# Kernel optimization log

Hardware: AMD Instinct MI355X
Metric: run time of the kernel (lower is better)

## Reference

```python
import jax, jax.numpy as jnp
import numpy as np

N = 50000      # nodes
E = 800000     # edges (avg degree 16)
IN = 128       # in_dim
OUT = 128      # out_dim
K = 4          # Chebyshev order
NEIG = 64      # num_eigs
H = 128        # eigval_hidden_dim
BN_EPS = 1e-5


def setup_inputs() -> dict:
    key = jax.random.key(0)
    ks = jax.random.split(key, 12)
    feature = jax.random.normal(ks[0], (N, IN), jnp.float32)
    # linear over concat of (K Chebyshev blocks + 1 spectral block) = (K+1)*IN
    lin_w = jax.random.normal(ks[1], ((K + 1) * IN, OUT), jnp.float32) / np.sqrt((K + 1) * IN)
    lin_b = jnp.zeros((OUT,), jnp.float32)
    # eigval_filter MLP: 1 -> H -> H -> 1 (ReLU between)
    ew0 = jax.random.normal(ks[2], (1, H), jnp.float32)
    eb0 = jnp.zeros((H,), jnp.float32)
    ew1 = jax.random.normal(ks[3], (H, H), jnp.float32) / np.sqrt(H)
    eb1 = jnp.zeros((H,), jnp.float32)
    ew2 = jax.random.normal(ks[4], (H, 1), jnp.float32) / np.sqrt(H)
    eb2 = jnp.zeros((1,), jnp.float32)
    bn_gamma = jnp.ones((OUT,), jnp.float32)
    bn_beta = jnp.zeros((OUT,), jnp.float32)
    lambda_max = jnp.ones((1,), jnp.float32)
    # cached (detached) spectral data for the graph
    evecs = jax.random.normal(ks[5], (N, NEIG), jnp.float32)
    evals = jax.random.uniform(ks[6], (NEIG,), jnp.float32)
    edge_src = jax.random.randint(ks[7], (E,), 0, N, jnp.int32).astype(jnp.int64)
    edge_dst = jax.random.randint(ks[8], (E,), 0, N, jnp.int32).astype(jnp.int64)
    return dict(feature=feature, lin_w=lin_w, lin_b=lin_b, ew0=ew0, eb0=eb0,
                ew1=ew1, eb1=eb1, ew2=ew2, eb2=eb2, bn_gamma=bn_gamma,
                bn_beta=bn_beta, lambda_max=lambda_max, evecs=evecs,
                evals=evals, edge_src=edge_src, edge_dst=edge_dst)


def reference(feature, lin_w, lin_b, ew0, eb0, ew1, eb1, ew2, eb2,
              bn_gamma, bn_beta, lambda_max, evecs, evals, edge_src, edge_dst):
    src = edge_src.astype(jnp.int32)
    dst = edge_dst.astype(jnp.int32)
    # in-degrees (messages arrive at dst) and D^-1/2, clamped at 1
    deg = jax.ops.segment_sum(jnp.ones((E,), jnp.float32), dst, num_segments=N)
    d_sqrt = jnp.clip(deg, 1.0, None) ** -0.5  # [N]
    d_sqrt = d_sqrt[:, None]                   # [N,1]

    def unn_laplacian(x):
        m = (x * d_sqrt)[src]                              # [E,IN]
        agg = jax.ops.segment_sum(m, dst, num_segments=N)  # [N,IN]
        return agg * d_sqrt

    re_norm = 2.0 / lambda_max  # broadcast scalar (per-node in dgl, constant here)

    X0 = feature
    blocks = [X0]
    h = unn_laplacian(X0)
    X1 = -re_norm * h + X0 * (re_norm - 1.0)
    blocks.append(X1)
    for _ in range(2, K):
        h = unn_laplacian(X1)
        Xi = -2.0 * re_norm * h + X1 * 2.0 * (re_norm - 1.0) - X0
        blocks.append(Xi)
        X1, X0 = Xi, X1

    # spectral filtering: evecs^T f, scale by MLP(evals), project back
    z = jax.nn.relu(evals[:, None] @ ew0 + eb0)   # [NEIG,H]
    z = jax.nn.relu(z @ ew1 + eb1)                # [NEIG,H]
    ef = z @ ew2 + eb2                            # [NEIG,1]
    hs = jnp.einsum('ne,nf->ef', evecs, feature)  # [NEIG,IN]
    hs = ef * hs
    hs = jnp.einsum('ne,ef->nf', evecs, hs)       # [N,IN]
    blocks.append(hs)

    Xt = jnp.concatenate(blocks, axis=1)          # [N,(K+1)*IN]
    out = Xt @ lin_w + lin_b                      # [N,OUT]

    # BatchNorm1d (training-mode batch statistics, biased variance)
    mu = jnp.mean(out, axis=0)
    var = jnp.mean((out - mu) ** 2, axis=0)
    out = (out - mu) * jax.lax.rsqrt(var + BN_EPS) * bn_gamma + bn_beta
    out = jax.nn.relu(out)
    # dropout p=0.0 -> identity; residual disabled
    return out
```

## Files before the change

kernel.cpp:

```cpp
#include <hip/hip_runtime.h>

#define N_NODES 50000
#define N_EDGES 800000
#define IN_F    128
#define OUT_F   128
#define NEIG    64
#define HDIM    128
#define BN_EPSF 1e-5f
#define XB_ROWS 50048
#define XB_COLS 640
#define SCAN_BLK 49
#define HSP_BLOCKS 521
#define HSP_NODES 96
#define RED_CHUNK 33
#define RED_SPLIT 16

typedef __attribute__((ext_vector_type(8))) short short8;
typedef __attribute__((ext_vector_type(4))) float floatx4;

#define OFF_XB      0
#define OFF_X1F     (XB_ROWS * XB_COLS / 2)
#define OFF_X2F     (OFF_X1F + N_NODES * IN_F)
#define OFF_WT      (OFF_X2F + N_NODES * IN_F)
#define OFF_DSQRT   (OFF_WT + 40960)
#define OFF_HS      (OFF_DSQRT + N_NODES)
#define OFF_EF      (OFF_HS + NEIG * OUT_F)
#define OFF_COLSUM  (OFF_EF + NEIG)
#define OFF_COLSQ   (OFF_COLSUM + OUT_F)
#define OFF_DEG     (OFF_COLSQ + OUT_F)
#define OFF_ROWSTART (OFF_DEG + N_NODES)
#define OFF_CSR     (OFF_ROWSTART + N_NODES + 1)
#define OFF_BSUM    (OFF_CSR + N_EDGES)
#define OFF_RANK    (OFF_BSUM + 64)

static __device__ inline unsigned short f2bf(float f) {
    union { float f; unsigned int u; } v; v.f = f;
    unsigned int r = (v.u + 0x7FFFu + ((v.u >> 16) & 1u)) >> 16;
    return (unsigned short)r;
}
static __device__ inline float bf2f(unsigned int u16) {
    union { unsigned int u; float f; } v; v.u = u16 << 16;
    return v.f;
}

__global__ __launch_bounds__(256) void k_prep(const float* __restrict__ feat,
                                              const float* __restrict__ W,
                                              unsigned short* __restrict__ Xb,
                                              unsigned short* __restrict__ Wt,
                                              int* __restrict__ deg,
                                              float* __restrict__ small) {
    int b = blockIdx.x;
    if (b < 3125) {
        int t = b * 256 + threadIdx.x;
        int n = t >> 4, c8 = (t & 15) * 8;
        float4 a = *(const float4*)&feat[n * IN_F + c8];
        float4 bb = *(const float4*)&feat[n * IN_F + c8 + 4];
        ushort4 o0, o1;
        o0.x = f2bf(a.x); o0.y = f2bf(a.y); o0.z = f2bf(a.z); o0.w = f2bf(a.w);
        o1.x = f2bf(bb.x); o1.y = f2bf(bb.y); o1.z = f2bf(bb.z); o1.w = f2bf(bb.w);
        *(ushort4*)&Xb[(size_t)n * XB_COLS + c8]     = o0;
        *(ushort4*)&Xb[(size_t)n * XB_COLS + c8 + 4] = o1;
    } else if (b < 3445) {
        int t = (b - 3125) * 256 + threadIdx.x;
        int k = t >> 7, n = t & 127;
        Wt[n * 640 + k] = f2bf(W[k * 128 + n]);
    } else {
        int i = (b - 3445) * 256 + threadIdx.x;
        if (i < N_NODES) deg[i] = 0;
        if (i < NEIG * OUT_F + NEIG + 2 * OUT_F) small[i] = 0.0f;
    }
}

__global__ void k_rank(int* __restrict__ deg, const int* __restrict__ dst,
                       int* __restrict__ rank) {
    int e = blockIdx.x * 256 + threadIdx.x;
    if (e < N_EDGES) rank[e] = atomicAdd(&deg[dst[e]], 1);
}

__global__ __launch_bounds__(1024) void k_scan1(const int* __restrict__ deg,
                                                int* __restrict__ row_start,
                                                int* __restrict__ bsum) {
    __shared__ int sd[1024];
    int i = blockIdx.x * 1024 + threadIdx.x;
    int v = (i < N_NODES) ? deg[i] : 0;
    sd[threadIdx.x] = v;
    __syncthreads();
    for (int off = 1; off < 1024; off <<= 1) {
        int t = (threadIdx.x >= off) ? sd[threadIdx.x - off] : 0;
        __syncthreads();
        sd[threadIdx.x] += t;
        __syncthreads();
    }
    if (i < N_NODES) row_start[i] = sd[threadIdx.x] - v;
    if (threadIdx.x == 1023) bsum[blockIdx.x] = sd[1023];
}

__global__ void k_scan2(int* __restrict__ bsum) {
    int t = threadIdx.x;
    int orig = (t < SCAN_BLK) ? bsum[t] : 0;
    int v = orig;
    for (int off = 1; off < 64; off <<= 1) {
        int u = __shfl_up(v, off);
        if (t >= off) v += u;
    }
    if (t < SCAN_BLK) bsum[t] = v - orig;
}

__global__ __launch_bounds__(1024) void k_scan3(const int* __restrict__ deg,
                                                int* __restrict__ row_start,
                                                const int* __restrict__ bsum,
                                                float* __restrict__ dsq) {
    int i = blockIdx.x * 1024 + threadIdx.x;
    if (i < N_NODES) {
        int r = row_start[i] + bsum[blockIdx.x];
        row_start[i] = r;
        dsq[i] = rsqrtf((float)max(deg[i], 1));
    }
    if (i == 0) row_start[N_NODES] = N_EDGES;
}

__global__ void k_csr(const int* __restrict__ src, const int* __restrict__ dst,
                      const int* __restrict__ rank, const int* __restrict__ row_start,
                      int* __restrict__ csr_src) {
    int e = blockIdx.x * 256 + threadIdx.x;
    if (e < N_EDGES) csr_src[row_start[dst[e]] + rank[e]] = src[e];
}

__global__ __launch_bounds__(256) void k_gather(const int* __restrict__ row_start,
                                                const int* __restrict__ csr_src,
                                                const float* __restrict__ dsq,
                                                const unsigned short* __restrict__ srcb,
                                                const unsigned short* __restrict__ prevb,
                                                const unsigned short* __restrict__ ppb,
                                                unsigned short* __restrict__ outb,
                                                const float* __restrict__ lm, int first) {
    int n = (blockIdx.x * 256 + threadIdx.x) >> 6;
    int lane = threadIdx.x & 63;
    if (n >= N_NODES) return;
    float rn = 2.0f / lm[0];
    float ax = 0.0f, ay = 0.0f;
    int beg = row_start[n], end = row_start[n + 1];
    int i = beg;
    for (; i + 8 <= end; i += 8) {
        int s0 = __builtin_amdgcn_readfirstlane(csr_src[i]);
        int s1 = __builtin_amdgcn_readfirstlane(csr_src[i + 1]);
        int s2 = __builtin_amdgcn_readfirstlane(csr_src[i + 2]);
        int s3 = __builtin_amdgcn_readfirstlane(csr_src[i + 3]);
        int s4 = __builtin_amdgcn_readfirstlane(csr_src[i + 4]);
        int s5 = __builtin_amdgcn_readfirstlane(csr_src[i + 5]);
        int s6 = __builtin_amdgcn_readfirstlane(csr_src[i + 6]);
        int s7 = __builtin_amdgcn_readfirstlane(csr_src[i + 7]);
        float c0 = dsq[s0], c1 = dsq[s1], c2 = dsq[s2], c3 = dsq[s3];
        float c4 = dsq[s4], c5 = dsq[s5], c6 = dsq[s6], c7 = dsq[s7];
        unsigned int p0 = *(const unsigned int*)&srcb[(size_t)s0 * XB_COLS + lane * 2];
        unsigned int p1 = *(const unsigned int*)&srcb[(size_t)s1 * XB_COLS + lane * 2];
        unsigned int p2 = *(const unsigned int*)&srcb[(size_t)s2 * XB_COLS + lane * 2];
        unsigned int p3 = *(const unsigned int*)&srcb[(size_t)s3 * XB_COLS + lane * 2];
        unsigned int p4 = *(const unsigned int*)&srcb[(size_t)s4 * XB_COLS + lane * 2];
        unsigned int p5 = *(const unsigned int*)&srcb[(size_t)s5 * XB_COLS + lane * 2];
        unsigned int p6 = *(const unsigned int*)&srcb[(size_t)s6 * XB_COLS + lane * 2];
        unsigned int p7 = *(const unsigned int*)&srcb[(size_t)s7 * XB_COLS + lane * 2];
        ax += c0 * bf2f(p0 & 0xffffu) + c1 * bf2f(p1 & 0xffffu)
            + c2 * bf2f(p2 & 0xffffu) + c3 * bf2f(p3 & 0xffffu)
            + c4 * bf2f(p4 & 0xffffu) + c5 * bf2f(p5 & 0xffffu)
            + c6 * bf2f(p6 & 0xffffu) + c7 * bf2f(p7 & 0xffffu);
        ay += c0 * bf2f(p0 >> 16) + c1 * bf2f(p1 >> 16)
            + c2 * bf2f(p2 >> 16) + c3 * bf2f(p3 >> 16)
            + c4 * bf2f(p4 >> 16) + c5 * bf2f(p5 >> 16)
            + c6 * bf2f(p6 >> 16) + c7 * bf2f(p7 >> 16);
    }
    for (; i + 4 <= end; i += 4) {
        int s0 = __builtin_amdgcn_readfirstlane(csr_src[i]);
        int s1 = __builtin_amdgcn_readfirstlane(csr_src[i + 1]);
        int s2 = __builtin_amdgcn_readfirstlane(csr_src[i + 2]);
        int s3 = __builtin_amdgcn_readfirstlane(csr_src[i + 3]);
        float c0 = dsq[s0], c1 = dsq[s1], c2 = dsq[s2], c3 = dsq[s3];
        unsigned int p0 = *(const unsigned int*)&srcb[(size_t)s0 * XB_COLS + lane * 2];
        unsigned int p1 = *(const unsigned int*)&srcb[(size_t)s1 * XB_COLS + lane * 2];
        unsigned int p2 = *(const unsigned int*)&srcb[(size_t)s2 * XB_COLS + lane * 2];
        unsigned int p3 = *(const unsigned int*)&srcb[(size_t)s3 * XB_COLS + lane * 2];
        ax += c0 * bf2f(p0 & 0xffffu) + c1 * bf2f(p1 & 0xffffu)
            + c2 * bf2f(p2 & 0xffffu) + c3 * bf2f(p3 & 0xffffu);
        ay += c0 * bf2f(p0 >> 16) + c1 * bf2f(p1 >> 16)
            + c2 * bf2f(p2 >> 16) + c3 * bf2f(p3 >> 16);
    }
    for (; i < end; ++i) {
        int s = __builtin_amdgcn_readfirstlane(csr_src[i]);
        float sc = dsq[s];
        unsigned int pv = *(const unsigned int*)&srcb[(size_t)s * XB_COLS + lane * 2];
        ax += sc * bf2f(pv & 0xffffu);
        ay += sc * bf2f(pv >> 16);
    }
    float ds = dsq[n];
    float a = (first ? -rn : -2.0f * rn) * ds;
    float b = first ? (rn - 1.0f) : 2.0f * (rn - 1.0f);
    unsigned int pu = *(const unsigned int*)&prevb[(size_t)n * XB_COLS + lane * 2];
    float rx = a * ax + b * bf2f(pu & 0xffffu);
    float ry = a * ay + b * bf2f(pu >> 16);
    if (ppb) {
        unsigned int qu = *(const unsigned int*)&ppb[(size_t)n * XB_COLS + lane * 2];
        rx -= bf2f(qu & 0xffffu);
        ry -= bf2f(qu >> 16);
    }
    unsigned int packed = (unsigned int)f2bf(rx) | ((unsigned int)f2bf(ry) << 16);
    *(unsigned int*)&outb[(size_t)n * XB_COLS + lane * 2] = packed;
}

__global__ __launch_bounds__(128) void k_ef2(const float* __restrict__ evals,
                                             const float* __restrict__ ew0,
                                             const float* __restrict__ eb0,
                                             const float* __restrict__ ew1,
                                             const float* __restrict__ eb1,
                                             const float* __restrict__ ew2,
                                             const float* __restrict__ eb2,
                                             float* __restrict__ ef) {
    __shared__ float z0[HDIM];
    __shared__ float red[HDIM];
    int i = blockIdx.x, j = threadIdx.x;
    float ev = evals[i];
    z0[j] = fmaxf(0.0f, ev * ew0[j] + eb0[j]);
    __syncthreads();
    float s0 = 0.f, s1 = 0.f, s2 = 0.f, s3 = 0.f;
    for (int h = 0; h < HDIM; h += 4) {
        s0 += z0[h]     * ew1[(h) * HDIM + j];
        s1 += z0[h + 1] * ew1[(h + 1) * HDIM + j];
        s2 += z0[h + 2] * ew1[(h + 2) * HDIM + j];
        s3 += z0[h + 3] * ew1[(h + 3) * HDIM + j];
    }
    float z1 = fmaxf(0.0f, eb1[j] + s0 + s1 + s2 + s3);
    red[j] = z1 * ew2[j];
    __syncthreads();
    for (int off = 64; off > 0; off >>= 1) {
        if (j < off) red[j] += red[j + off];
        __syncthreads();
    }
    if (j == 0) ef[i] = red[0] + eb2[0];
}

__global__ __launch_bounds__(256) void k_hs_partial2(const float* __restrict__ evecs,
                                                     const float* __restrict__ feat,
                                                     float* __restrict__ partials) {
    __shared__ float sEv[32 * NEIG];
    __shared__ float sFt[32 * IN_F];
    int t = threadIdx.x;
    int e0 = (t >> 5) * 8;
    int f0 = (t & 31) * 4;
    float acc[8][4];
#pragma unroll
    for (int r = 0; r < 8; ++r)
#pragma unroll
        for (int c = 0; c < 4; ++c) acc[r][c] = 0.0f;

    int n0 = blockIdx.x * HSP_NODES;
    for (int ch = 0; ch < HSP_NODES; ch += 32) {
        int base = n0 + ch;
        {
            int r = t >> 3, c = (t & 7) * 8;
            int n = base + r;
            float4 a, b;
            if (n < N_NODES) {
                a = *(const float4*)&evecs[(size_t)n * NEIG + c];
                b = *(const float4*)&evecs[(size_t)n * NEIG + c + 4];
            } else {
                a = make_float4(0, 0, 0, 0); b = a;
            }
            *(float4*)&sEv[r * NEIG + c] = a;
            *(float4*)&sEv[r * NEIG + c + 4] = b;
        }
        {
            int r = t >> 3, c = (t & 7) * 16;
            int n = base + r;
#pragma unroll
            for (int q = 0; q < 4; ++q) {
                float4 v = (n < N_NODES) ? *(const float4*)&feat[(size_t)n * IN_F + c + q * 4]
                                         : make_float4(0, 0, 0, 0);
                *(float4*)&sFt[r * IN_F + c + q * 4] = v;
            }
        }
        __syncthreads();
#pragma unroll 2
        for (int i = 0; i < 32; ++i) {
            float4 ev0 = *(float4*)&sEv[i * NEIG + e0];
            float4 ev1 = *(float4*)&sEv[i * NEIG + e0 + 4];
            float4 fv  = *(float4*)&sFt[i * IN_F + f0];
            float evv[8] = {ev0.x, ev0.y, ev0.z, ev0.w, ev1.x, ev1.y, ev1.z, ev1.w};
#pragma unroll
            for (int r = 0; r < 8; ++r) {
                acc[r][0] += evv[r] * fv.x;
                acc[r][1] += evv[r] * fv.y;
                acc[r][2] += evv[r] * fv.z;
                acc[r][3] += evv[r] * fv.w;
            }
        }
        __syncthreads();
    }
    float* p = &partials[(size_t)blockIdx.x * (NEIG * IN_F)];
#pragma unroll
    for (int r = 0; r < 8; ++r)
        *(float4*)&p[(e0 + r) * IN_F + f0] = make_float4(acc[r][0], acc[r][1], acc[r][2], acc[r][3]);
}

__global__ __launch_bounds__(256) void k_hs_reduce(const float* __restrict__ partials,
                                                   float* __restrict__ hs_small) {
    int grp   = blockIdx.x & 31;
    int chunk = blockIdx.x >> 5;
    int idx = grp * 256 + threadIdx.x;
    int j0 = chunk * RED_CHUNK;
    int j1 = min(j0 + RED_CHUNK, HSP_BLOCKS);
    float s = 0.0f;
    for (int j = j0; j < j1; ++j) s += partials[(size_t)j * (NEIG * IN_F) + idx];
    atomicAdd(&hs_small[idx], s);
}

__global__ __launch_bounds__(256) void k_hs_apply2(unsigned short* __restrict__ Xb,
                                                   const float* __restrict__ evecs,
                                                   const float* __restrict__ hs_small,
                                                   const float* __restrict__ ef) {
    __shared__ float sShs[NEIG * HDIM];
    __shared__ float sEv[32 * NEIG];
    int t = threadIdx.x;
    int n0 = blockIdx.x * 32;
    {
        float efv = ef[t >> 2];
        int pbase = t * 32;
#pragma unroll
        for (int q = 0; q < 8; ++q) {
            float4 v = *(const float4*)&hs_small[pbase + q * 4];
            v.x *= efv; v.y *= efv; v.z *= efv; v.w *= efv;
            *(float4*)&sShs[pbase + q * 4] = v;
        }
    }
    {
        int r = t >> 3, c = (t & 7) * 8;
        int n = n0 + r;
        float4 a, b;
        if (n < N_NODES) {
            a = *(const float4*)&evecs[(size_t)n * NEIG + c];
            b = *(const float4*)&evecs[(size_t)n * NEIG + c + 4];
        } else {
            a = make_float4(0, 0, 0, 0); b = a;
        }
        *(float4*)&sEv[r * NEIG + c] = a;
        *(float4*)&sEv[r * NEIG + c + 4] = b;
    }
    __syncthreads();
    int nb = (t >> 5) * 4;
    int f0 = (t & 31) * 4;
    float acc[4][4];
#pragma unroll
    for (int q = 0; q < 4; ++q)
#pragma unroll
        for (int c = 0; c < 4; ++c) acc[q][c] = 0.0f;
    for (int e = 0; e < NEIG; ++e) {
        float4 sv = *(float4*)&sShs[e * HDIM + f0];
#pragma unroll
        for (int q = 0; q < 4; ++q) {
            float evv = sEv[(nb + q) * NEIG + e];
            acc[q][0] += evv * sv.x;
            acc[q][1] += evv * sv.y;
            acc[q][2] += evv * sv.z;
            acc[q][3] += evv * sv.w;
        }
    }
#pragma unroll
    for (int q = 0; q < 4; ++q) {
        int n = n0 + nb + q;
        if (n < N_NODES) {
            ushort4 o;
            o.x = f2bf(acc[q][0]); o.y = f2bf(acc[q][1]);
            o.z = f2bf(acc[q][2]); o.w = f2bf(acc[q][3]);
            *(ushort4*)&Xb[(size_t)n * XB_COLS + 4 * IN_F + f0] = o;
        }
    }
}

__global__ __launch_bounds__(256) void k_gemm(const unsigned short* __restrict__ Xb,
                                              const unsigned short* __restrict__ Wt,
                                              const float* __restrict__ bias,
                                              float* __restrict__ out,
                                              float* __restrict__ colsum,
                                              float* __restrict__ colsq) {
    __shared__ unsigned short sA[128 * 32];
    __shared__ unsigned short sB[128 * 32];
    __shared__ float cs[4][OUT_F];
    __shared__ float cq[4][OUT_F];
    int tid = threadIdx.x;
    int wave = tid >> 6, lane = tid & 63;
    int quad = lane >> 4, m16 = lane & 15;
    int row0 = blockIdx.x * 128;

    floatx4 acc[2][8];
#pragma unroll
    for (int mt = 0; mt < 2; ++mt)
#pragma unroll
        for (int nt = 0; nt < 8; ++nt) acc[mt][nt] = (floatx4)(0.0f);

    int r  = tid >> 2;
    int c8 = (tid & 3) * 8;
    int gr0 = min(row0 + r, N_NODES - 1);
    int gr1 = min(row0 + r + 64, N_NODES - 1);

    for (int k0 = 0; k0 < 640; k0 += 32) {
        *(uint4*)&sA[r * 32 + c8]        = *(const uint4*)&Xb[(size_t)gr0 * XB_COLS + k0 + c8];
        *(uint4*)&sA[(r + 64) * 32 + c8] = *(const uint4*)&Xb[(size_t)gr1 * XB_COLS + k0 + c8];
        *(uint4*)&sB[r * 32 + c8]        = *(const uint4*)&Wt[r * 640 + k0 + c8];
        *(uint4*)&sB[(r + 64) * 32 + c8] = *(const uint4*)&Wt[(r + 64) * 640 + k0 + c8];
        __syncthreads();
        short8 a0 = *(short8*)&sA[(wave * 32 + m16) * 32 + quad * 8];
        short8 a1 = *(short8*)&sA[(wave * 32 + 16 + m16) * 32 + quad * 8];
#pragma unroll
        for (int nt = 0; nt < 8; ++nt) {
            short8 b = *(short8*)&sB[(nt * 16 + m16) * 32 + quad * 8];
            acc[0][nt] = __builtin_amdgcn_mfma_f32_16x16x32_bf16(a0, b, acc[0][nt], 0, 0, 0);
            acc[1][nt] = __builtin_amdgcn_mfma_f32_16x16x32_bf16(a1, b, acc[1][nt], 0, 0, 0);
        }
        __syncthreads();
    }
#pragma unroll
    for (int nt = 0; nt < 8; ++nt) {
        int col = nt * 16 + m16;
        float bb = bias[col];
        float sv = 0.0f, sq = 0.0f;
#pragma unroll
        for (int mt = 0; mt < 2; ++mt) {
            int rbase = row0 + wave * 32 + mt * 16 + quad * 4;
#pragma unroll
            for (int reg = 0; reg < 4; ++reg) {
                int row = rbase + reg;
                if (row < N_NODES) {
                    float w = acc[mt][nt][reg] + bb;
                    out[(size_t)row * OUT_F + col] = w;
                    sv += w;
                    sq += w * w;
                }
            }
        }
        sv += __shfl_down(sv, 32); sq += __shfl_down(sq, 32);
        sv += __shfl_down(sv, 16); sq += __shfl_down(sq, 16);
        if (lane < 16) { cs[wave][col] = sv; cq[wave][col] = sq; }
    }
    __syncthreads();
    if (tid < OUT_F) {
        float s = cs[0][tid] + cs[1][tid] + cs[2][tid] + cs[3][tid];
        float q = cq[0][tid] + cq[1][tid] + cq[2][tid] + cq[3][tid];
        atomicAdd(&colsum[tid], s);
        atomicAdd(&colsq[tid], q);
    }
}

__global__ void k_bn_apply(float* __restrict__ out, const float* __restrict__ colsum,
                           const float* __restrict__ colsq, const float* __restrict__ gamma,
                           const float* __restrict__ beta) {
    int t = blockIdx.x * 256 + threadIdx.x;
    int n = t >> 5, c = t & 31;
    float4 v = *(float4*)&out[n * OUT_F + c * 4];
    float4 s = *(const float4*)&colsum[c * 4];
    float4 q = *(const float4*)&colsq[c * 4];
    float4 g = *(const float4*)&gamma[c * 4];
    float4 b = *(const float4*)&beta[c * 4];
    const float invN = 1.0f / (float)N_NODES;
    float mux = s.x * invN, muy = s.y * invN, muz = s.z * invN, muw = s.w * invN;
    float ix = rsqrtf(q.x * invN - mux * mux + BN_EPSF);
    float iy = rsqrtf(q.y * invN - muy * muy + BN_EPSF);
    float iz = rsqrtf(q.z * invN - muz * muz + BN_EPSF);
    float iw = rsqrtf(q.w * invN - muw * muw + BN_EPSF);
    v.x = fmaxf(0.0f, (v.x - mux) * ix * g.x + b.x);
    v.y = fmaxf(0.0f, (v.y - muy) * iy * g.y + b.y);
    v.z = fmaxf(0.0f, (v.z - muz) * iz * g.z + b.z);
    v.w = fmaxf(0.0f, (v.w - muw) * iw * g.w + b.w);
    *(float4*)&out[n * OUT_F + c * 4] = v;
}

extern "C" void kernel_launch(void* const* d_in, const int* in_sizes, int n_in,
                              void* d_out, int out_size, void* d_ws, size_t ws_size,
                              hipStream_t stream) {
    const float* feature    = (const float*)d_in[0];
    const float* lin_w      = (const float*)d_in[1];
    const float* lin_b      = (const float*)d_in[2];
    const float* ew0        = (const float*)d_in[3];
    const float* eb0        = (const float*)d_in[4];
    const float* ew1        = (const float*)d_in[5];
    const float* eb1        = (const float*)d_in[6];
    const float* ew2        = (const float*)d_in[7];
    const float* eb2        = (const float*)d_in[8];
    const float* bn_gamma   = (const float*)d_in[9];
    const float* bn_beta    = (const float*)d_in[10];
    const float* lambda_max = (const float*)d_in[11];
    const float* evecs      = (const float*)d_in[12];
    const float* evals      = (const float*)d_in[13];
    const int*   edge_src   = (const int*)d_in[14];
    const int*   edge_dst   = (const int*)d_in[15];

    float* out = (float*)d_out;
    float* ws  = (float*)d_ws;
    unsigned short* Xb = (unsigned short*)(ws + OFF_XB);
    unsigned short* Wt = (unsigned short*)(ws + OFF_WT);
    float* dsq      = ws + OFF_DSQRT;
    float* hs_small = ws + OFF_HS;
    float* ef       = ws + OFF_EF;
    float* colsum   = ws + OFF_COLSUM;
    float* colsq    = ws + OFF_COLSQ;
    int*   deg      = (int*)(ws + OFF_DEG);
    int*   row_start= (int*)(ws + OFF_ROWSTART);
    int*   csr_src  = (int*)(ws + OFF_CSR);
    int*   bsum     = (int*)(ws + OFF_BSUM);
    int*   rank     = (int*)(ws + OFF_RANK);
    float* partials = ws + OFF_X1F;

    k_prep<<<3674, 256, 0, stream>>>(feature, lin_w, Xb, Wt, deg, hs_small);
    k_rank<<<(N_EDGES + 255) / 256, 256, 0, stream>>>(deg, edge_dst, rank);
    k_scan1<<<SCAN_BLK, 1024, 0, stream>>>(deg, row_start, bsum);
    k_scan2<<<1, 64, 0, stream>>>(bsum);
    k_scan3<<<SCAN_BLK, 1024, 0, stream>>>(deg, row_start, bsum, dsq);
    k_csr<<<(N_EDGES + 255) / 256, 256, 0, stream>>>(edge_src, edge_dst, rank, row_start, csr_src);

    const int GBLK = (N_NODES * 64 + 255) / 256;
    k_gather<<<GBLK, 256, 0, stream>>>(row_start, csr_src, dsq,
                                       Xb + 0, Xb + 0, (const unsigned short*)nullptr,
                                       Xb + IN_F, lambda_max, 1);
    k_gather<<<GBLK, 256, 0, stream>>>(row_start, csr_src, dsq,
                                       Xb + IN_F, Xb + IN_F, Xb + 0,
                                       Xb + 2 * IN_F, lambda_max, 0);
    k_gather<<<GBLK, 256, 0, stream>>>(row_start, csr_src, dsq,
                                       Xb + 2 * IN_F, Xb + 2 * IN_F, Xb + IN_F,
                                       Xb + 3 * IN_F, lambda_max, 0);

    k_ef2<<<NEIG, 128, 0, stream>>>(evals, ew0, eb0, ew1, eb1, ew2, eb2, ef);
    k_hs_partial2<<<HSP_BLOCKS, 256, 0, stream>>>(evecs, feature, partials);
    k_hs_reduce<<<32 * RED_SPLIT, 256, 0, stream>>>(partials, hs_small);
    k_hs_apply2<<<(N_NODES + 31) / 32, 256, 0, stream>>>(Xb, evecs, hs_small, ef);

    k_gemm<<<(N_NODES + 127) / 128, 256, 0, stream>>>(Xb, Wt, lin_b, out, colsum, colsq);
    k_bn_apply<<<(N_NODES * 32) / 256, 256, 0, stream>>>(out, colsum, colsq, bn_gamma, bn_beta);
}
```

Measured before the change: 369.9 us.

## Slice feature matrix into 32-column panels and gather per XCC-local slice

Replaces the row-major [N,640] bf16 concat buffer with 20 column slices of [N,32], so each gather pass touches a compact 3.2 MB panel that can stay resident in one XCC's L2. The gather kernels become persistent 2048-block launches that pull 16-node chunks from per-slice atomic cursors, with each XCC starting on a different slice. Each wave now splits edges across 4 lane groups with a shuffle reduction and uses nontemporal loads and stores. The GEMM and spectral kernels are updated to read and write the sliced layout. The gain relies on cache locality per XCC, in exchange for atomic cursor traffic, more passes over row_start and csr_src, and reliance on the XCC_ID hardware register.

```diff
diff --git a/kernel.cpp b/kernel.cpp
--- a/kernel.cpp
+++ b/kernel.cpp
@@ -7,31 +7,33 @@
 #define NEIG    64
 #define HDIM    128
 #define BN_EPSF 1e-5f
-#define XB_ROWS 50048
-#define XB_COLS 640
 #define SCAN_BLK 49
 #define HSP_BLOCKS 521
 #define HSP_NODES 96
 #define RED_CHUNK 33
 #define RED_SPLIT 16
+#define NCHUNKS 3125
+#define GATHER_BLOCKS 2048
 
 typedef __attribute__((ext_vector_type(8))) short short8;
 typedef __attribute__((ext_vector_type(4))) float floatx4;
 
-#define OFF_XB      0
-#define OFF_X1F     (XB_ROWS * XB_COLS / 2)
-#define OFF_X2F     (OFF_X1F + N_NODES * IN_F)
-#define OFF_WT      (OFF_X2F + N_NODES * IN_F)
+#define N32        ((size_t)N_NODES * 32)
+#define OFF_XS      0
+#define OFF_PART    16000000
+#define OFF_WT      (OFF_PART + HSP_BLOCKS * 8192)
 #define OFF_DSQRT   (OFF_WT + 40960)
 #define OFF_HS      (OFF_DSQRT + N_NODES)
-#define OFF_EF      (OFF_HS + NEIG * OUT_F)
+#define OFF_EF      (OFF_HS + 8192)
 #define OFF_COLSUM  (OFF_EF + NEIG)
 #define OFF_COLSQ   (OFF_COLSUM + OUT_F)
-#define OFF_DEG     (OFF_COLSQ + OUT_F)
+#define OFF_CUR     (OFF_COLSQ + OUT_F)
+#define OFF_DEG     (OFF_CUR + 16)
 #define OFF_ROWSTART (OFF_DEG + N_NODES)
 #define OFF_CSR     (OFF_ROWSTART + N_NODES + 1)
 #define OFF_BSUM    (OFF_CSR + N_EDGES)
 #define OFF_RANK    (OFF_BSUM + 64)
+#define ZERO_SMALL  (8192 + NEIG + 2 * OUT_F + 16)
 
 static __device__ inline unsigned short f2bf(float f) {
     union { float f; unsigned int u; } v; v.f = f;
@@ -45,7 +47,7 @@
 
 __global__ __launch_bounds__(256) void k_prep(const float* __restrict__ feat,
                                               const float* __restrict__ W,
-                                              unsigned short* __restrict__ Xb,
+                                              unsigned short* __restrict__ XS,
                                               unsigned short* __restrict__ Wt,
                                               int* __restrict__ deg,
                                               float* __restrict__ small) {
@@ -58,8 +60,10 @@
         ushort4 o0, o1;
         o0.x = f2bf(a.x); o0.y = f2bf(a.y); o0.z = f2bf(a.z); o0.w = f2bf(a.w);
         o1.x = f2bf(bb.x); o1.y = f2bf(bb.y); o1.z = f2bf(bb.z); o1.w = f2bf(bb.w);
-        *(ushort4*)&Xb[(size_t)n * XB_COLS + c8]     = o0;
-        *(ushort4*)&Xb[(size_t)n * XB_COLS + c8 + 4] = o1;
+        int slice = c8 >> 5, within = c8 & 31;
+        unsigned short* p = XS + (size_t)slice * N32 + (size_t)n * 32 + within;
+        *(ushort4*)p = o0;
+        *(ushort4*)(p + 4) = o1;
     } else if (b < 3445) {
         int t = (b - 3125) * 256 + threadIdx.x;
         int k = t >> 7, n = t & 127;
@@ -67,7 +71,7 @@
     } else {
         int i = (b - 3445) * 256 + threadIdx.x;
         if (i < N_NODES) deg[i] = 0;
-        if (i < NEIG * OUT_F + NEIG + 2 * OUT_F) small[i] = 0.0f;
+        if (i < ZERO_SMALL) small[i] = 0.0f;
     }
 }
 
@@ -129,81 +133,77 @@
 __global__ __launch_bounds__(256) void k_gather(const int* __restrict__ row_start,
                                                 const int* __restrict__ csr_src,
                                                 const float* __restrict__ dsq,
-                                                const unsigned short* __restrict__ srcb,
-                                                const unsigned short* __restrict__ prevb,
-                                                const unsigned short* __restrict__ ppb,
-                                                unsigned short* __restrict__ outb,
-                                                const float* __restrict__ lm, int first) {
-    int n = (blockIdx.x * 256 + threadIdx.x) >> 6;
+                                                unsigned short* __restrict__ XS,
+                                                const float* __restrict__ lm,
+                                                int first, int srcC, int ppC, int outC,
+                                                int* __restrict__ cursors) {
+    int xcc;
+    asm volatile("s_getreg_b32 %0, hwreg(HW_REG_XCC_ID)" : "=s"(xcc));
+    int wv = threadIdx.x >> 6;
     int lane = threadIdx.x & 63;
-    if (n >= N_NODES) return;
+    int g = lane >> 4, fl = lane & 15;
     float rn = 2.0f / lm[0];
-    float ax = 0.0f, ay = 0.0f;
-    int beg = row_start[n], end = row_start[n + 1];
-    int i = beg;
-    for (; i + 8 <= end; i += 8) {
-        int s0 = __builtin_amdgcn_readfirstlane(csr_src[i]);
-        int s1 = __builtin_amdgcn_readfirstlane(csr_src[i + 1]);
-        int s2 = __builtin_amdgcn_readfirstlane(csr_src[i + 2]);
-        int s3 = __builtin_amdgcn_readfirstlane(csr_src[i + 3]);
-        int s4 = __builtin_amdgcn_readfirstlane(csr_src[i + 4]);
-        int s5 = __builtin_amdgcn_readfirstlane(csr_src[i + 5]);
-        int s6 = __builtin_amdgcn_readfirstlane(csr_src[i + 6]);
-        int s7 = __builtin_amdgcn_readfirstlane(csr_src[i + 7]);
-        float c0 = dsq[s0], c1 = dsq[s1], c2 = dsq[s2], c3 = dsq[s3];
-        float c4 = dsq[s4], c5 = dsq[s5], c6 = dsq[s6], c7 = dsq[s7];
-        unsigned int p0 = *(const unsigned int*)&srcb[(size_t)s0 * XB_COLS + lane * 2];
-        unsigned int p1 = *(const unsigned int*)&srcb[(size_t)s1 * XB_COLS + lane * 2];
-        unsigned int p2 = *(const unsigned int*)&srcb[(size_t)s2 * XB_COLS + lane * 2];
-        unsigned int p3 = *(const unsigned int*)&srcb[(size_t)s3 * XB_COLS + lane * 2];
-        unsigned int p4 = *(const unsigned int*)&srcb[(size_t)s4 * XB_COLS + lane * 2];
-        unsigned int p5 = *(const unsigned int*)&srcb[(size_t)s5 * XB_COLS + lane * 2];
-        unsigned int p6 = *(const unsigned int*)&srcb[(size_t)s6 * XB_COLS + lane * 2];
-        unsigned int p7 = *(const unsigned int*)&srcb[(size_t)s7 * XB_COLS + lane * 2];
-        ax += c0 * bf2f(p0 & 0xffffu) + c1 * bf2f(p1 & 0xffffu)
-            + c2 * bf2f(p2 & 0xffffu) + c3 * bf2f(p3 & 0xffffu)
-            + c4 * bf2f(p4 & 0xffffu) + c5 * bf2f(p5 & 0xffffu)
-            + c6 * bf2f(p6 & 0xffffu) + c7 * bf2f(p7 & 0xffffu);
-        ay += c0 * bf2f(p0 >> 16) + c1 * bf2f(p1 >> 16)
-            + c2 * bf2f(p2 >> 16) + c3 * bf2f(p3 >> 16)
-            + c4 * bf2f(p4 >> 16) + c5 * bf2f(p5 >> 16)
-            + c6 * bf2f(p6 >> 16) + c7 * bf2f(p7 >> 16);
-    }
-    for (; i + 4 <= end; i += 4) {
-        int s0 = __builtin_amdgcn_readfirstlane(csr_src[i]);
-        int s1 = __builtin_amdgcn_readfirstlane(csr_src[i + 1]);
-        int s2 = __builtin_amdgcn_readfirstlane(csr_src[i + 2]);
-        int s3 = __builtin_amdgcn_readfirstlane(csr_src[i + 3]);
-        float c0 = dsq[s0], c1 = dsq[s1], c2 = dsq[s2], c3 = dsq[s3];
-        unsigned int p0 = *(const unsigned int*)&srcb[(size_t)s0 * XB_COLS + lane * 2];
-        unsigned int p1 = *(const unsigned int*)&srcb[(size_t)s1 * XB_COLS + lane * 2];
-        unsigned int p2 = *(const unsigned int*)&srcb[(size_t)s2 * XB_COLS + lane * 2];
-        unsigned int p3 = *(const unsigned int*)&srcb[(size_t)s3 * XB_COLS + lane * 2];
-        ax += c0 * bf2f(p0 & 0xffffu) + c1 * bf2f(p1 & 0xffffu)
-            + c2 * bf2f(p2 & 0xffffu) + c3 * bf2f(p3 & 0xffffu);
-        ay += c0 * bf2f(p0 >> 16) + c1 * bf2f(p1 >> 16)
-            + c2 * bf2f(p2 >> 16) + c3 * bf2f(p3 >> 16);
-    }
-    for (; i < end; ++i) {
-        int s = __builtin_amdgcn_readfirstlane(csr_src[i]);
-        float sc = dsq[s];
-        unsigned int pv = *(const unsigned int*)&srcb[(size_t)s * XB_COLS + lane * 2];
-        ax += sc * bf2f(pv & 0xffffu);
-        ay += sc * bf2f(pv >> 16);
-    }
-    float ds = dsq[n];
-    float a = (first ? -rn : -2.0f * rn) * ds;
-    float b = first ? (rn - 1.0f) : 2.0f * (rn - 1.0f);
-    unsigned int pu = *(const unsigned int*)&prevb[(size_t)n * XB_COLS + lane * 2];
-    float rx = a * ax + b * bf2f(pu & 0xffffu);
-    float ry = a * ay + b * bf2f(pu >> 16);
-    if (ppb) {
-        unsigned int qu = *(const unsigned int*)&ppb[(size_t)n * XB_COLS + lane * 2];
-        rx -= bf2f(qu & 0xffffu);
-        ry -= bf2f(qu >> 16);
-    }
-    unsigned int packed = (unsigned int)f2bf(rx) | ((unsigned int)f2bf(ry) << 16);
-    *(unsigned int*)&outb[(size_t)n * XB_COLS + lane * 2] = packed;
+    float bcoef = first ? (rn - 1.0f) : 2.0f * (rn - 1.0f);
+    float am = first ? -rn : -2.0f * rn;
+    __shared__ int s_chunk;
+
+    for (int pass = 0; pass < 4; ++pass) {
+        int slice = (xcc + pass) & 3;
+        const unsigned short* srcS = XS + (size_t)(srcC + slice) * N32;
+        const unsigned short* ppS  = (ppC >= 0) ? XS + (size_t)(ppC + slice) * N32 : nullptr;
+        unsigned short* outS = XS + (size_t)(outC + slice) * N32;
+        int* cur = &cursors[slice];
+        while (true) {
+            __syncthreads();
+            if (threadIdx.x == 0) s_chunk = atomicAdd(cur, 1);
+            __syncthreads();
+            int chunk = s_chunk;
+            if (chunk >= NCHUNKS) break;
+            int nbase = chunk * 16 + wv * 4;
+#pragma unroll
+            for (int k = 0; k < 4; ++k) {
+                int n = nbase + k;
+                int beg = row_start[n], end = row_start[n + 1];
+                float ax = 0.0f, ay = 0.0f;
+                int i = beg;
+                for (; i + 8 <= end; i += 8) {
+                    int s0 = __builtin_nontemporal_load(&csr_src[i + g]);
+                    int s1 = __builtin_nontemporal_load(&csr_src[i + 4 + g]);
+                    float c0 = dsq[s0], c1 = dsq[s1];
+                    unsigned int p0 = *(const unsigned int*)&srcS[(size_t)s0 * 32 + fl * 2];
+                    unsigned int p1 = *(const unsigned int*)&srcS[(size_t)s1 * 32 + fl * 2];
+                    ax += c0 * bf2f(p0 & 0xffffu) + c1 * bf2f(p1 & 0xffffu);
+                    ay += c0 * bf2f(p0 >> 16) + c1 * bf2f(p1 >> 16);
+                }
+                for (; i < end; i += 4) {
+                    int idx = i + g;
+                    bool act = idx < end;
+                    int s0 = act ? __builtin_nontemporal_load(&csr_src[idx]) : 0;
+                    float c0 = act ? dsq[s0] : 0.0f;
+                    unsigned int p0 = *(const unsigned int*)&srcS[(size_t)s0 * 32 + fl * 2];
+                    ax += c0 * bf2f(p0 & 0xffffu);
+                    ay += c0 * bf2f(p0 >> 16);
+                }
+                ax += __shfl_down(ax, 32); ay += __shfl_down(ay, 32);
+                ax += __shfl_down(ax, 16); ay += __shfl_down(ay, 16);
+                if (lane < 16) {
+                    float a = am * dsq[n];
+                    unsigned int pu = *(const unsigned int*)&srcS[(size_t)n * 32 + fl * 2];
+                    float rx = a * ax + bcoef * bf2f(pu & 0xffffu);
+                    float ry = a * ay + bcoef * bf2f(pu >> 16);
+                    if (ppS) {
+                        unsigned int qu = __builtin_nontemporal_load(
+                            (const unsigned int*)&ppS[(size_t)n * 32 + fl * 2]);
+                        rx -= bf2f(qu & 0xffffu);
+                        ry -= bf2f(qu >> 16);
+                    }
+                    unsigned int packed = (unsigned int)f2bf(rx) | ((unsigned int)f2bf(ry) << 16);
+                    __builtin_nontemporal_store(packed,
+                        (unsigned int*)&outS[(size_t)n * 32 + fl * 2]);
+                }
+            }
+        }
+    }
 }
 
 __global__ __launch_bounds__(128) void k_ef2(const float* __restrict__ evals,
@@ -312,7 +312,7 @@
     atomicAdd(&hs_small[idx], s);
 }
 
-__global__ __launch_bounds__(256) void k_hs_apply2(unsigned short* __restrict__ Xb,
+__global__ __launch_bounds__(256) void k_hs_apply2(unsigned short* __restrict__ XS,
                                                    const float* __restrict__ evecs,
                                                    const float* __restrict__ hs_small,
                                                    const float* __restrict__ ef) {
@@ -362,6 +362,8 @@
             acc[q][3] += evv * sv.w;
         }
     }
+    unsigned short* outc = XS + (size_t)(16 + (f0 >> 5)) * N32;
+    int within = f0 & 31;
 #pragma unroll
     for (int q = 0; q < 4; ++q) {
         int n = n0 + nb + q;
@@ -369,12 +371,12 @@
             ushort4 o;
             o.x = f2bf(acc[q][0]); o.y = f2bf(acc[q][1]);
             o.z = f2bf(acc[q][2]); o.w = f2bf(acc[q][3]);
-            *(ushort4*)&Xb[(size_t)n * XB_COLS + 4 * IN_F + f0] = o;
-        }
-    }
-}
-
-__global__ __launch_bounds__(256) void k_gemm(const unsigned short* __restrict__ Xb,
+            *(ushort4*)&outc[(size_t)n * 32 + within] = o;
+        }
+    }
+}
+
+__global__ __launch_bounds__(256) void k_gemm(const unsigned short* __restrict__ XS,
                                               const unsigned short* __restrict__ Wt,
                                               const float* __restrict__ bias,
                                               float* __restrict__ out,
@@ -401,8 +403,9 @@
     int gr1 = min(row0 + r + 64, N_NODES - 1);
 
     for (int k0 = 0; k0 < 640; k0 += 32) {
-        *(uint4*)&sA[r * 32 + c8]        = *(const uint4*)&Xb[(size_t)gr0 * XB_COLS + k0 + c8];
-        *(uint4*)&sA[(r + 64) * 32 + c8] = *(const uint4*)&Xb[(size_t)gr1 * XB_COLS + k0 + c8];
+        const unsigned short* base = XS + (size_t)(k0 >> 5) * N32;
+        *(uint4*)&sA[r * 32 + c8]        = *(const uint4*)&base[(size_t)gr0 * 32 + c8];
+        *(uint4*)&sA[(r + 64) * 32 + c8] = *(const uint4*)&base[(size_t)gr1 * 32 + c8];
         *(uint4*)&sB[r * 32 + c8]        = *(const uint4*)&Wt[r * 640 + k0 + c8];
         *(uint4*)&sB[(r + 64) * 32 + c8] = *(const uint4*)&Wt[(r + 64) * 640 + k0 + c8];
         __syncthreads();
@@ -493,43 +496,40 @@
 
     float* out = (float*)d_out;
     float* ws  = (float*)d_ws;
-    unsigned short* Xb = (unsigned short*)(ws + OFF_XB);
+    unsigned short* XS = (unsigned short*)(ws + OFF_XS);
+    float* partials = ws + OFF_PART;
     unsigned short* Wt = (unsigned short*)(ws + OFF_WT);
     float* dsq      = ws + OFF_DSQRT;
     float* hs_small = ws + OFF_HS;
     float* ef       = ws + OFF_EF;
     float* colsum   = ws + OFF_COLSUM;
     float* colsq    = ws + OFF_COLSQ;
+    int*   cursors  = (int*)(ws + OFF_CUR);
     int*   deg      = (int*)(ws + OFF_DEG);
     int*   row_start= (int*)(ws + OFF_ROWSTART);
     int*   csr_src  = (int*)(ws + OFF_CSR);
     int*   bsum     = (int*)(ws + OFF_BSUM);
     int*   rank     = (int*)(ws + OFF_RANK);
-    float* partials = ws + OFF_X1F;
-
-    k_prep<<<3674, 256, 0, stream>>>(feature, lin_w, Xb, Wt, deg, hs_small);
+
+    k_prep<<<3674, 256, 0, stream>>>(feature, lin_w, XS, Wt, deg, ws + OFF_HS);
     k_rank<<<(N_EDGES + 255) / 256, 256, 0, stream>>>(deg, edge_dst, rank);
     k_scan1<<<SCAN_BLK, 1024, 0, stream>>>(deg, row_start, bsum);
     k_scan2<<<1, 64, 0, stream>>>(bsum);
     k_scan3<<<SCAN_BLK, 1024, 0, stream>>>(deg, row_start, bsum, dsq);
     k_csr<<<(N_EDGES + 255) / 256, 256, 0, stream>>>(edge_src, edge_dst, rank, row_start, csr_src);
 
-    const int GBLK = (N_NODES * 64 + 255) / 256;
-    k_gather<<<GBLK, 256, 0, stream>>>(row_start, csr_src, dsq,
-                                       Xb + 0, Xb + 0, (const unsigned short*)nullptr,
-                                       Xb + IN_F, lambda_max, 1);
-    k_gather<<<GBLK, 256, 0, stream>>>(row_start, csr_src, dsq,
-                                       Xb + IN_F, Xb + IN_F, Xb + 0,
-                                       Xb + 2 * IN_F, lambda_max, 0);
-    k_gather<<<GBLK, 256, 0, stream>>>(row_start, csr_src, dsq,
-                                       Xb + 2 * IN_F, Xb + 2 * IN_F, Xb + IN_F,
-                                       Xb + 3 * IN_F, lambda_max, 0);
+    k_gather<<<GATHER_BLOCKS, 256, 0, stream>>>(row_start, csr_src, dsq, XS, lambda_max,
+                                                1, 0, -1, 4, cursors + 0);
+    k_gather<<<GATHER_BLOCKS, 256, 0, stream>>>(row_start, csr_src, dsq, XS, lambda_max,
+                                                0, 4, 0, 8, cursors + 4);
+    k_gather<<<GATHER_BLOCKS, 256, 0, stream>>>(row_start, csr_src, dsq, XS, lambda_max,
+                                                0, 8, 4, 12, cursors + 8);
 
     k_ef2<<<NEIG, 128, 0, stream>>>(evals, ew0, eb0, ew1, eb1, ew2, eb2, ef);
     k_hs_partial2<<<HSP_BLOCKS, 256, 0, stream>>>(evecs, feature, partials);
     k_hs_reduce<<<32 * RED_SPLIT, 256, 0, stream>>>(partials, hs_small);
-    k_hs_apply2<<<(N_NODES + 31) / 32, 256, 0, stream>>>(Xb, evecs, hs_small, ef);
-
-    k_gemm<<<(N_NODES + 127) / 128, 256, 0, stream>>>(Xb, Wt, lin_b, out, colsum, colsq);
+    k_hs_apply2<<<(N_NODES + 31) / 32, 256, 0, stream>>>(XS, evecs, hs_small, ef);
+
+    k_gemm<<<(N_NODES + 127) / 128, 256, 0, stream>>>(XS, Wt, lin_b, out, colsum, colsq);
     k_bn_apply<<<(N_NODES * 32) / 256, 256, 0, stream>>>(out, colsum, colsq, bn_gamma, bn_beta);
 }
```

After: 1.032 ms. 179% more time.
